# Kernel tuning notes

Hardware: AMD Instinct MI355X
Metric: run time of the kernel (lower is better)

## Reference

```python
import jax, jax.numpy as jnp
import numpy as np

# Dimensions (config.* values chosen per shape_source)
B, T, V = 64, 128, 512          # batch, seq_len, vocabnum (input feature dim)
H = 512                          # NUM_HIDDEN_UNITS
A = 64                           # ATTENTION_SIZE
C = 500                          # ClassEmbeddingsize
EPS = 1e-5


def _layer_norm(z, g, b):
    m = jnp.mean(z, axis=-1, keepdims=True)
    v = jnp.mean(jnp.square(z - m), axis=-1, keepdims=True)
    return (z - m) * jax.lax.rsqrt(v + EPS) * g + b


def _lstm_dir(x, w_ih, w_hh, ln_g, ln_b):
    # x: [T,B,D]; w_ih: [4H,D]; w_hh: [4H,H]; ln_g/ln_b: [9H] -> (ih 4H, hh 4H, cell H)
    g_ih, g_hh, g_c = ln_g[:4 * H], ln_g[4 * H:8 * H], ln_g[8 * H:]
    b_ih, b_hh, b_c = ln_b[:4 * H], ln_b[4 * H:8 * H], ln_b[8 * H:]
    # precompute input contribution for all steps, layer-normed over gate dim
    xg = _layer_norm(jnp.einsum('tbd,gd->tbg', x, w_ih), g_ih, b_ih)  # [T,B,4H]

    def step(carry, xg_t):
        h, c = carry
        gates = xg_t + _layer_norm(h @ w_hh.T, g_hh, b_hh)  # [B,4H]
        i, f, g, o = jnp.split(gates, 4, axis=-1)
        c = jax.nn.sigmoid(f) * c + jax.nn.sigmoid(i) * jnp.tanh(g)
        h = jax.nn.sigmoid(o) * jnp.tanh(_layer_norm(c, g_c, b_c))
        return (h, c), h

    h0 = jnp.zeros((x.shape[1], H), x.dtype)
    (_, _), hs = jax.lax.scan(step, (h0, h0), xg)
    return hs  # [T,B,H]


def _bilstm_layer(x, w_ih, w_hh, ln_g, ln_b):
    # direction-stacked params: w_ih [2,4H,D], w_hh [2,4H,H], ln_* [2,9H]
    fwd = _lstm_dir(x, w_ih[0], w_hh[0], ln_g[0], ln_b[0])
    bwd = _lstm_dir(x[::-1], w_ih[1], w_hh[1], ln_g[1], ln_b[1])[::-1]
    return jnp.concatenate([fwd, bwd], axis=-1)  # [T,B,2H]


def _batchnorm(x, g, b):
    # x: [B,C,L]; training-mode batch statistics over (B,L)
    m = jnp.mean(x, axis=(0, 2), keepdims=True)
    v = jnp.mean(jnp.square(x - m), axis=(0, 2), keepdims=True)
    return (x - m) * jax.lax.rsqrt(v + EPS) * g[None, :, None] + b[None, :, None]


def setup_inputs() -> dict:
    key = jax.random.key(0)
    ks = jax.random.split(key, 12)
    rn = lambda k, s: jax.random.normal(k, s, jnp.float32) * 0.05
    return {
        'batch_embedded': jax.random.normal(ks[0], (B, T, V), jnp.float32),
        'bn1_g': jnp.ones((V,), jnp.float32), 'bn1_b': jnp.zeros((V,), jnp.float32),
        'bn2_g': jnp.ones((2 * H,), jnp.float32), 'bn2_b': jnp.zeros((2 * H,), jnp.float32),
        'w_ih0': rn(ks[1], (2, 4 * H, V)), 'w_hh0': rn(ks[2], (2, 4 * H, H)),
        'lng0': jnp.ones((2, 9 * H), jnp.float32), 'lnb0': jnp.zeros((2, 9 * H), jnp.float32),
        'w_ih1': rn(ks[3], (2, 4 * H, 2 * H)), 'w_hh1': rn(ks[4], (2, 4 * H, H)),
        'lng1': jnp.ones((2, 9 * H), jnp.float32), 'lnb1': jnp.zeros((2, 9 * H), jnp.float32),
        'w_omega': rn(ks[5], (2 * H, A)), 'b_omega': rn(ks[6], (A,)), 'u_omega': rn(ks[7], (A,)),
        'W': jax.random.uniform(ks[8], (2 * H + 1, C + 1), jnp.float32) * 0.05,
    }


def reference(batch_embedded, bn1_g, bn1_b, bn2_g, bn2_b,
              w_ih0, w_hh0, lng0, lnb0, w_ih1, w_hh1, lng1, lnb1,
              w_omega, b_omega, u_omega, W):
    # BatchNorm1d over feature channels (dropout = identity in eval)
    x = _batchnorm(jnp.transpose(batch_embedded, (0, 2, 1)), bn1_g, bn1_b)  # [B,V,T]
    x = jnp.transpose(x, (2, 0, 1))  # [T,B,V]
    # 2-layer bidirectional layer-norm LSTM
    x = _bilstm_layer(x, w_ih0, w_hh0, lng0, lnb0)   # [T,B,2H]
    x = _bilstm_layer(x, w_ih1, w_hh1, lng1, lnb1)   # [T,B,2H]
    x = _batchnorm(jnp.transpose(x, (1, 2, 0)), bn2_g, bn2_b)  # [B,2H,T]
    x = jnp.transpose(x, (0, 2, 1))  # [B,T,2H]
    # Attention pooling over time
    v = jnp.tanh(x @ w_omega + b_omega)              # [B,T,A]
    alphas = jax.nn.softmax(v @ u_omega, axis=1)     # [B,T]
    pooled = jnp.sum(x * alphas[..., None], axis=1)  # [B,2H]
    emb = jnp.pad(pooled, ((0, 0), (0, 1)), constant_values=1.0)  # [B,2H+1]
    return emb @ W  # [B,C+1]
```

## Files before the change

kernel.cpp:

```cpp
#include <hip/hip_runtime.h>
#include <hip/hip_bf16.h>

#define LN_EPS 1e-5f

using bf16x8 = __attribute__((ext_vector_type(8))) short;
using f32x4  = __attribute__((ext_vector_type(4))) float;

__device__ __forceinline__ float bf2f(ushort u) {
    union { unsigned int i; float f; } v; v.i = ((unsigned int)u) << 16; return v.f;
}
__device__ __forceinline__ ushort f2bf(float f) {
    union { unsigned int i; float f; } v; v.f = f;
    unsigned int r = v.i + 0x7FFFu + ((v.i >> 16) & 1u);
    return (ushort)(r >> 16);
}
__device__ __forceinline__ void split3(float x, ushort& a, ushort& b, ushort& c) {
    a = f2bf(x); float r = x - bf2f(a);
    b = f2bf(r); float r2 = r - bf2f(b);
    c = f2bf(r2);
}

__device__ __forceinline__ unsigned ld_flag(const unsigned* p) {
    return __hip_atomic_load(p, __ATOMIC_RELAXED, __HIP_MEMORY_SCOPE_AGENT);
}
__device__ __forceinline__ void st_flag(unsigned* p, unsigned v) {
    __hip_atomic_store(p, v, __ATOMIC_RELAXED, __HIP_MEMORY_SCOPE_AGENT);
}

__device__ __forceinline__ void blockReduceSum2(float& a, float& b, float* red) {
    #pragma unroll
    for (int off = 32; off > 0; off >>= 1) {
        a += __shfl_down(a, off, 64);
        b += __shfl_down(b, off, 64);
    }
    const int nw = blockDim.x >> 6;
    const int w = threadIdx.x >> 6;
    if ((threadIdx.x & 63) == 0) { red[2 * w] = a; red[2 * w + 1] = b; }
    __syncthreads();
    if (threadIdx.x == 0) {
        float sa = 0.f, sb = 0.f;
        for (int i = 0; i < nw; ++i) { sa += red[2 * i]; sb += red[2 * i + 1]; }
        red[10] = sa; red[11] = sb;
    }
    __syncthreads();
    a = red[10]; b = red[11];
    __syncthreads();
}

__global__ __launch_bounds__(256) void conv_split3_k(const float* __restrict__ src, ushort* __restrict__ d0,
                                                     ushort* __restrict__ d1, ushort* __restrict__ d2, int n4) {
    int i = blockIdx.x * 256 + threadIdx.x;
    if (i < n4) {
        float4 v = ((const float4*)src)[i];
        ushort4 a, b, c;
        split3(v.x, a.x, b.x, c.x); split3(v.y, a.y, b.y, c.y);
        split3(v.z, a.z, b.z, c.z); split3(v.w, a.w, b.w, c.w);
        ((ushort4*)d0)[i] = a; ((ushort4*)d1)[i] = b; ((ushort4*)d2)[i] = c;
    }
}

__global__ __launch_bounds__(256) void bn1_stats_k(const float* __restrict__ in, float* __restrict__ st) {
    int b = blockIdx.x, tid = threadIdx.x;
    float s10 = 0, s20 = 0, s11 = 0, s21 = 0;
    const float* p = in + (size_t)b * 128 * 512;
    for (int t = 0; t < 128; ++t) {
        float x0 = p[t * 512 + tid];
        float x1 = p[t * 512 + tid + 256];
        s10 += x0; s20 += x0 * x0; s11 += x1; s21 += x1 * x1;
    }
    atomicAdd(&st[tid], s10);       atomicAdd(&st[512 + tid], s20);
    atomicAdd(&st[tid + 256], s11); atomicAdd(&st[512 + tid + 256], s21);
}

__global__ void bn1_final_k(const float* __restrict__ st, const float* __restrict__ g,
                            const float* __restrict__ bb, float* __restrict__ ac) {
    int d = threadIdx.x + blockIdx.x * 256;
    if (d < 512) {
        float m = st[d] * (1.f / 8192.f);
        float v = st[512 + d] * (1.f / 8192.f) - m * m;
        float a = g[d] * rsqrtf(v + LN_EPS);
        ac[d] = a; ac[512 + d] = bb[d] - m * a;
    }
}

__global__ __launch_bounds__(128) void bn1_apply3_k(const float* __restrict__ in, const float* __restrict__ ac,
                                                    ushort* __restrict__ x0, ushort* __restrict__ x1,
                                                    ushort* __restrict__ x2) {
    int beta = blockIdx.x;
    int t = beta >> 6, b = beta & 63;
    const float* src = in + ((size_t)b * 128 + t) * 512;
    #pragma unroll
    for (int k = 0; k < 4; ++k) {
        int d = threadIdx.x + 128 * k;
        ushort a, m, l;
        split3(ac[d] * src[d] + ac[512 + d], a, m, l);
        x0[(size_t)beta * 512 + d] = a;
        x1[(size_t)beta * 512 + d] = m;
        x2[(size_t)beta * 512 + d] = l;
    }
}

__global__ __launch_bounds__(256) void gemm6_k(const ushort* __restrict__ A0, const ushort* __restrict__ A1,
                                               const ushort* __restrict__ A2,
                                               const ushort* __restrict__ W0, const ushort* __restrict__ W1,
                                               const ushort* __restrict__ W2,
                                               float* __restrict__ C, int K) {
    const int dir = blockIdx.z;
    const ushort* Wp0 = W0 + (size_t)dir * 2048 * K;
    const ushort* Wp1 = W1 + (size_t)dir * 2048 * K;
    const ushort* Wp2 = W2 + (size_t)dir * 2048 * K;
    const int wave = threadIdx.x >> 6, lane = threadIdx.x & 63;
    const int l15 = lane & 15, kq = lane >> 4;
    const int m0 = blockIdx.y * 128 + (wave >> 1) * 64;
    const int n0 = blockIdx.x * 128 + (wave & 1) * 64;
    f32x4 acc[4][4];
    #pragma unroll
    for (int i = 0; i < 4; ++i)
        #pragma unroll
        for (int j = 0; j < 4; ++j) acc[i][j] = (f32x4){0.f, 0.f, 0.f, 0.f};
    for (int k0 = 0; k0 < K; k0 += 32) {
        bf16x8 a0[4], a1[4], a2[4], b0[4], b1[4], b2[4];
        #pragma unroll
        for (int i = 0; i < 4; ++i) {
            size_t o = (size_t)(m0 + i * 16 + l15) * K + k0 + kq * 8;
            a0[i] = *(const bf16x8*)(A0 + o);
            a1[i] = *(const bf16x8*)(A1 + o);
            a2[i] = *(const bf16x8*)(A2 + o);
        }
        #pragma unroll
        for (int j = 0; j < 4; ++j) {
            size_t o = (size_t)(n0 + j * 16 + l15) * K + k0 + kq * 8;
            b0[j] = *(const bf16x8*)(Wp0 + o);
            b1[j] = *(const bf16x8*)(Wp1 + o);
            b2[j] = *(const bf16x8*)(Wp2 + o);
        }
        #pragma unroll
        for (int i = 0; i < 4; ++i)
            #pragma unroll
            for (int j = 0; j < 4; ++j) {
                acc[i][j] = __builtin_amdgcn_mfma_f32_16x16x32_bf16(a2[i], b0[j], acc[i][j], 0, 0, 0);
                acc[i][j] = __builtin_amdgcn_mfma_f32_16x16x32_bf16(a1[i], b1[j], acc[i][j], 0, 0, 0);
                acc[i][j] = __builtin_amdgcn_mfma_f32_16x16x32_bf16(a0[i], b2[j], acc[i][j], 0, 0, 0);
                acc[i][j] = __builtin_amdgcn_mfma_f32_16x16x32_bf16(a1[i], b0[j], acc[i][j], 0, 0, 0);
                acc[i][j] = __builtin_amdgcn_mfma_f32_16x16x32_bf16(a0[i], b1[j], acc[i][j], 0, 0, 0);
                acc[i][j] = __builtin_amdgcn_mfma_f32_16x16x32_bf16(a0[i], b0[j], acc[i][j], 0, 0, 0);
            }
    }
    #pragma unroll
    for (int i = 0; i < 4; ++i)
        #pragma unroll
        for (int j = 0; j < 4; ++j)
            #pragma unroll
            for (int r = 0; r < 4; ++r)
                C[(size_t)dir * 8192 * 2048 + (size_t)(m0 + i * 16 + kq * 4 + r) * 2048 + n0 + j * 16 + l15]
                    = acc[i][j][r];
}

__global__ __launch_bounds__(256) void ln_rows32_k(float* __restrict__ X, const float* __restrict__ lng,
                                                   const float* __restrict__ lnb) {
    __shared__ float red[12];
    const int dir = blockIdx.y;
    float* row = X + ((size_t)dir * 8192 + blockIdx.x) * 2048;
    const float* g = lng + dir * 4608;
    const float* bb = lnb + dir * 4608;
    const int tid = threadIdx.x;
    float4 v0 = ((const float4*)row)[tid], v1 = ((const float4*)row)[tid + 256];
    float s1 = v0.x + v0.y + v0.z + v0.w + v1.x + v1.y + v1.z + v1.w;
    float s2 = v0.x * v0.x + v0.y * v0.y + v0.z * v0.z + v0.w * v0.w
             + v1.x * v1.x + v1.y * v1.y + v1.z * v1.z + v1.w * v1.w;
    blockReduceSum2(s1, s2, red);
    float m = s1 * (1.f / 2048.f);
    float rs = rsqrtf(s2 * (1.f / 2048.f) - m * m + LN_EPS);
    float4 g0 = ((const float4*)g)[tid],  g1 = ((const float4*)g)[tid + 256];
    float4 b0 = ((const float4*)bb)[tid], b1 = ((const float4*)bb)[tid + 256];
    float4 o0, o1;
    o0.x = (v0.x - m) * rs * g0.x + b0.x; o0.y = (v0.y - m) * rs * g0.y + b0.y;
    o0.z = (v0.z - m) * rs * g0.z + b0.z; o0.w = (v0.w - m) * rs * g0.w + b0.w;
    o1.x = (v1.x - m) * rs * g1.x + b1.x; o1.y = (v1.y - m) * rs * g1.y + b1.y;
    o1.z = (v1.z - m) * rs * g1.z + b1.z; o1.w = (v1.w - m) * rs * g1.w + b1.w;
    ((float4*)row)[tid] = o0;
    ((float4*)row)[tid + 256] = o1;
}

__device__ __forceinline__ void gbar3(unsigned int* flags, unsigned int e) {
    __builtin_amdgcn_s_waitcnt(0);
    __syncthreads();
    if (threadIdx.x == 0) {
        __builtin_amdgcn_fence(__ATOMIC_RELEASE, "agent");
        st_flag(&flags[blockIdx.x * 16], e);
    }
    if (threadIdx.x < 128) {
        while (ld_flag(&flags[threadIdx.x * 16]) < e)
            __builtin_amdgcn_s_sleep(2);
    }
    __syncthreads();
    __builtin_amdgcn_fence(__ATOMIC_ACQUIRE, "agent");
}

__global__ __launch_bounds__(256, 1) void lstm_scan5_k(
    const float* __restrict__ xg,
    const ushort* __restrict__ w0, const ushort* __restrict__ w1, const ushort* __restrict__ w2,
    const float* __restrict__ lng, const float* __restrict__ lnb,
    ushort* __restrict__ hb0, ushort* __restrict__ hb1, ushort* __restrict__ hb2,
    float* __restrict__ graw,
    ushort* __restrict__ hs0, ushort* __restrict__ hs1, ushort* __restrict__ hs2,
    unsigned int* __restrict__ flags) {
    __shared__ float red[12];
    const int beta = blockIdx.x, tid = threadIdx.x;
    const int dirB = beta >> 6, bB = beta & 63;
    const int wave = tid >> 6, lane = tid & 63, l15 = lane & 15, kq = lane >> 4;
    const size_t hro = (size_t)(dirB * 64 + bB) * 512;
    ((unsigned*)(hb0 + hro))[tid] = 0u;
    ((unsigned*)(hb1 + hro))[tid] = 0u;
    ((unsigned*)(hb2 + hro))[tid] = 0u;
    float c0 = 0.f, c1 = 0.f;
    const float* g_hh = lng + dirB * 4608 + 2048;
    const float* b_hh = lnb + dirB * 4608 + 2048;
    const float2 gcv = ((const float2*)(lng + dirB * 4608 + 4096))[tid];
    const float2 bcv = ((const float2*)(lnb + dirB * 4608 + 4096))[tid];
    const int jj = wave >> 1, ip = wave & 1;
    const int nn = bB * 32 + jj * 16;
    const ushort* h0d = hb0 + (size_t)dirB * 64 * 512;
    const ushort* h1d = hb1 + (size_t)dirB * 64 * 512;
    const ushort* h2d = hb2 + (size_t)dirB * 64 * 512;
    float* gr = graw + dirB * 64 * 2048;
    bf16x8 wr[16][3];
    {
        const ushort* w0d = w0 + (size_t)dirB * 2048 * 512;
        const ushort* w1d = w1 + (size_t)dirB * 2048 * 512;
        const ushort* w2d = w2 + (size_t)dirB * 2048 * 512;
        #pragma unroll
        for (int kt = 0; kt < 16; ++kt) {
            size_t wo = (size_t)(nn + l15) * 512 + kt * 32 + kq * 8;
            wr[kt][0] = *(const bf16x8*)(w0d + wo);
            wr[kt][1] = *(const bf16x8*)(w1d + wo);
            wr[kt][2] = *(const bf16x8*)(w2d + wo);
        }
    }
    unsigned int e = 0;
    gbar3(flags, ++e);
    for (int s = 0; s < 128; ++s) {
        {
            f32x4 acc[2];
            acc[0] = (f32x4){0.f, 0.f, 0.f, 0.f};
            acc[1] = (f32x4){0.f, 0.f, 0.f, 0.f};
            #pragma unroll
            for (int kt = 0; kt < 16; ++kt) {
                #pragma unroll
                for (int ii = 0; ii < 2; ++ii) {
                    size_t ho = (size_t)(ip * 32 + ii * 16 + l15) * 512 + kt * 32 + kq * 8;
                    bf16x8 a0 = *(const bf16x8*)(h0d + ho);
                    bf16x8 a1 = *(const bf16x8*)(h1d + ho);
                    bf16x8 a2 = *(const bf16x8*)(h2d + ho);
                    acc[ii] = __builtin_amdgcn_mfma_f32_16x16x32_bf16(a2, wr[kt][0], acc[ii], 0, 0, 0);
                    acc[ii] = __builtin_amdgcn_mfma_f32_16x16x32_bf16(a1, wr[kt][1], acc[ii], 0, 0, 0);
                    acc[ii] = __builtin_amdgcn_mfma_f32_16x16x32_bf16(a0, wr[kt][2], acc[ii], 0, 0, 0);
                    acc[ii] = __builtin_amdgcn_mfma_f32_16x16x32_bf16(a1, wr[kt][0], acc[ii], 0, 0, 0);
                    acc[ii] = __builtin_amdgcn_mfma_f32_16x16x32_bf16(a0, wr[kt][1], acc[ii], 0, 0, 0);
                    acc[ii] = __builtin_amdgcn_mfma_f32_16x16x32_bf16(a0, wr[kt][0], acc[ii], 0, 0, 0);
                }
            }
            #pragma unroll
            for (int ii = 0; ii < 2; ++ii)
                #pragma unroll
                for (int r = 0; r < 4; ++r)
                    gr[(ip * 32 + ii * 16 + kq * 4 + r) * 2048 + nn + l15] = acc[ii][r];
        }
        gbar3(flags, ++e);
        {
            const int time = dirB ? (127 - s) : s;
            const float2* grow = (const float2*)(gr + bB * 2048);
            float v[8];
            #pragma unroll
            for (int j = 0; j < 4; ++j) {
                float2 g2 = grow[j * 256 + tid];
                v[2 * j] = g2.x; v[2 * j + 1] = g2.y;
            }
            float s1 = 0.f, s2 = 0.f;
            #pragma unroll
            for (int k = 0; k < 8; ++k) { s1 += v[k]; s2 += v[k] * v[k]; }
            blockReduceSum2(s1, s2, red);
            float mu = s1 * (1.f / 2048.f);
            float rs = rsqrtf(s2 * (1.f / 2048.f) - mu * mu + LN_EPS);
            const float2* xr = (const float2*)(xg + ((size_t)dirB * 8192 + (size_t)time * 64 + bB) * 2048);
            float nv[8];
            #pragma unroll
            for (int j = 0; j < 4; ++j) {
                float2 xv = xr[tid + 256 * j];
                float2 gh = ((const float2*)g_hh)[tid + 256 * j];
                float2 bh = ((const float2*)b_hh)[tid + 256 * j];
                nv[2 * j]     = xv.x + (v[2 * j]     - mu) * rs * gh.x + bh.x;
                nv[2 * j + 1] = xv.y + (v[2 * j + 1] - mu) * rs * gh.y + bh.y;
            }
            float si0 = 1.f / (1.f + expf(-nv[0])), si1 = 1.f / (1.f + expf(-nv[1]));
            float sf0 = 1.f / (1.f + expf(-nv[2])), sf1 = 1.f / (1.f + expf(-nv[3]));
            c0 = sf0 * c0 + si0 * tanhf(nv[4]);
            c1 = sf1 * c1 + si1 * tanhf(nv[5]);
            float t1 = c0 + c1, t2 = c0 * c0 + c1 * c1;
            blockReduceSum2(t1, t2, red);
            float mc = t1 * (1.f / 512.f);
            float rc = rsqrtf(t2 * (1.f / 512.f) - mc * mc + LN_EPS);
            float so0 = 1.f / (1.f + expf(-nv[6])), so1 = 1.f / (1.f + expf(-nv[7]));
            float h0v = so0 * tanhf((c0 - mc) * rc * gcv.x + bcv.x);
            float h1v = so1 * tanhf((c1 - mc) * rc * gcv.y + bcv.y);
            ushort a0, m0, l0, a1, m1, l1;
            split3(h0v, a0, m0, l0);
            split3(h1v, a1, m1, l1);
            unsigned p0 = (unsigned)a0 | ((unsigned)a1 << 16);
            unsigned p1 = (unsigned)m0 | ((unsigned)m1 << 16);
            unsigned p2 = (unsigned)l0 | ((unsigned)l1 << 16);
            ((unsigned*)(hb0 + hro))[tid] = p0;
            ((unsigned*)(hb1 + hro))[tid] = p1;
            ((unsigned*)(hb2 + hro))[tid] = p2;
            size_t oro = ((size_t)time * 64 + bB) * 1024 + dirB * 512;
            ((unsigned*)(hs0 + oro))[tid] = p0;
            ((unsigned*)(hs1 + oro))[tid] = p1;
            ((unsigned*)(hs2 + oro))[tid] = p2;
        }
        gbar3(flags, ++e);
    }
}

__global__ __launch_bounds__(256) void bn2_stats3_k(const ushort* __restrict__ h0, const ushort* __restrict__ h1,
                                                    const ushort* __restrict__ h2, float* __restrict__ st) {
    int t = blockIdx.x, tid = threadIdx.x;
    float s1[4] = {0, 0, 0, 0}, s2[4] = {0, 0, 0, 0};
    size_t base = (size_t)t * 64 * 1024;
    for (int b = 0; b < 64; ++b) {
        #pragma unroll
        for (int k = 0; k < 4; ++k) {
            size_t o = base + b * 1024 + tid + 256 * k;
            float x = bf2f(h0[o]) + bf2f(h1[o]) + bf2f(h2[o]);
            s1[k] += x; s2[k] += x * x;
        }
    }
    #pragma unroll
    for (int k = 0; k < 4; ++k) {
        atomicAdd(&st[tid + 256 * k], s1[k]);
        atomicAdd(&st[1024 + tid + 256 * k], s2[k]);
    }
}

__global__ void bn2_final_k(const float* __restrict__ st, const float* __restrict__ g,
                            const float* __restrict__ bb, float* __restrict__ ac) {
    #pragma unroll
    for (int k = 0; k < 4; ++k) {
        int h = threadIdx.x + 256 * k;
        float m = st[h] * (1.f / 8192.f);
        float v = st[1024 + h] * (1.f / 8192.f) - m * m;
        float a = g[h] * rsqrtf(v + LN_EPS);
        ac[h] = a; ac[1024 + h] = bb[h] - m * a;
    }
}

__global__ __launch_bounds__(256) void bn2_apply3_k(const ushort* __restrict__ h0, const ushort* __restrict__ h1,
                                                    const ushort* __restrict__ h2, const float* __restrict__ ac,
                                                    float* __restrict__ y) {
    int beta = blockIdx.x;
    int b = beta >> 7, t = beta & 127;
    size_t so = ((size_t)t * 64 + b) * 1024;
    float* dst = y + (size_t)beta * 1024;
    #pragma unroll
    for (int k = 0; k < 4; ++k) {
        int h = threadIdx.x + 256 * k;
        float x = bf2f(h0[so + h]) + bf2f(h1[so + h]) + bf2f(h2[so + h]);
        dst[h] = ac[h] * x + ac[1024 + h];
    }
}

__global__ __launch_bounds__(64) void att_scores_k(const float* __restrict__ y, const float* __restrict__ wo,
                                                   const float* __restrict__ bo, const float* __restrict__ uo,
                                                   float* __restrict__ sc) {
    int row = blockIdx.x;
    int a = threadIdx.x;
    const float* yr = y + (size_t)row * 1024;
    float acc = bo[a];
    for (int h = 0; h < 1024; h += 4) {
        float4 yv = *(const float4*)(yr + h);
        acc += yv.x * wo[(h + 0) * 64 + a];
        acc += yv.y * wo[(h + 1) * 64 + a];
        acc += yv.z * wo[(h + 2) * 64 + a];
        acc += yv.w * wo[(h + 3) * 64 + a];
    }
    float p = tanhf(acc) * uo[a];
    #pragma unroll
    for (int off = 32; off > 0; off >>= 1) p += __shfl_down(p, off, 64);
    if (a == 0) sc[row] = p;
}

__global__ __launch_bounds__(128) void att_softmax_k(const float* __restrict__ sc, float* __restrict__ al) {
    __shared__ float red[8];
    int b = blockIdx.x, t = threadIdx.x;
    int lane = t & 63, w = t >> 6;
    float v = sc[b * 128 + t];
    float m = v;
    #pragma unroll
    for (int off = 32; off > 0; off >>= 1) m = fmaxf(m, __shfl_down(m, off, 64));
    if (lane == 0) red[w] = m;
    __syncthreads();
    m = fmaxf(red[0], red[1]);
    float e = expf(v - m);
    float sum = e;
    #pragma unroll
    for (int off = 32; off > 0; off >>= 1) sum += __shfl_down(sum, off, 64);
    if (lane == 0) red[2 + w] = sum;
    __syncthreads();
    sum = red[2] + red[3];
    al[b * 128 + t] = e / sum;
}

__global__ __launch_bounds__(256) void att_pool_k(const float* __restrict__ y, const float* __restrict__ al,
                                                  float* __restrict__ pooled) {
    int b = blockIdx.x, tid = threadIdx.x;
    float acc[4] = {0, 0, 0, 0};
    const float* yb = y + (size_t)b * 128 * 1024;
    for (int t = 0; t < 128; ++t) {
        float a = al[b * 128 + t];
        #pragma unroll
        for (int k = 0; k < 4; ++k) acc[k] += a * yb[t * 1024 + tid + 256 * k];
    }
    #pragma unroll
    for (int k = 0; k < 4; ++k) pooled[b * 1024 + tid + 256 * k] = acc[k];
}

__global__ __launch_bounds__(256) void out_gemv_k(const float* __restrict__ pooled, const float* __restrict__ W,
                                                  float* __restrict__ out) {
    int b = blockIdx.x, tid = threadIdx.x;
    const float* pb = pooled + b * 1024;
    #pragma unroll
    for (int rep = 0; rep < 2; ++rep) {
        int c = tid + rep * 256;
        if (c < 501) {
            float acc = W[(size_t)1024 * 501 + c];
            for (int h = 0; h < 1024; ++h) acc += pb[h] * W[(size_t)h * 501 + c];
            out[b * 501 + c] = acc;
        }
    }
}

extern "C" void kernel_launch(void* const* d_in, const int* in_sizes, int n_in,
                              void* d_out, int out_size, void* d_ws, size_t ws_size,
                              hipStream_t stream) {
    (void)in_sizes; (void)n_in; (void)out_size; (void)ws_size;
    const float* in_x  = (const float*)d_in[0];
    const float* bn1g  = (const float*)d_in[1];
    const float* bn1b  = (const float*)d_in[2];
    const float* bn2g  = (const float*)d_in[3];
    const float* bn2b  = (const float*)d_in[4];
    const float* w_ih0 = (const float*)d_in[5];
    const float* w_hh0 = (const float*)d_in[6];
    const float* lng0  = (const float*)d_in[7];
    const float* lnb0  = (const float*)d_in[8];
    const float* w_ih1 = (const float*)d_in[9];
    const float* w_hh1 = (const float*)d_in[10];
    const float* lng1  = (const float*)d_in[11];
    const float* lnb1  = (const float*)d_in[12];
    const float* w_om  = (const float*)d_in[13];
    const float* b_om  = (const float*)d_in[14];
    const float* u_om  = (const float*)d_in[15];
    const float* Wf    = (const float*)d_in[16];
    float* out = (float*)d_out;

    char* ws = (char*)d_ws;
    size_t off = 0;
    auto alloc = [&](size_t bytes) { size_t o = off; off += (bytes + 255) & ~(size_t)255; return o; };
    float*  xg     = (float*)(ws + alloc(2ull * 8192 * 2048 * 4));
    ushort* hs0_0  = (ushort*)(ws + alloc(8192ull * 1024 * 2));
    ushort* hs0_1  = (ushort*)(ws + alloc(8192ull * 1024 * 2));
    ushort* hs0_2  = (ushort*)(ws + alloc(8192ull * 1024 * 2));
    char*   hs1reg = ws + alloc(3ull * 8192 * 1024 * 2);
    ushort* WH1_0  = (ushort*)(ws + alloc(2ull * 2048 * 512 * 2));
    ushort* WH1_1  = (ushort*)(ws + alloc(2ull * 2048 * 512 * 2));
    ushort* WH1_2  = (ushort*)(ws + alloc(2ull * 2048 * 512 * 2));
    float*  graw   = (float*)(ws + alloc(2ull * 64 * 2048 * 4));
    ushort* hb0    = (ushort*)(ws + alloc(2ull * 64 * 512 * 2));
    ushort* hb1    = (ushort*)(ws + alloc(2ull * 64 * 512 * 2));
    ushort* hb2    = (ushort*)(ws + alloc(2ull * 64 * 512 * 2));
    float*  st1    = (float*)(ws + alloc(1024 * 4));
    float*  ac1    = (float*)(ws + alloc(1024 * 4));
    float*  st2    = (float*)(ws + alloc(2048 * 4));
    float*  ac2    = (float*)(ws + alloc(2048 * 4));
    float*  sc     = (float*)(ws + alloc(8192 * 4));
    float*  al     = (float*)(ws + alloc(8192 * 4));
    float*  pooled = (float*)(ws + alloc(64ull * 1024 * 4));
    unsigned int* bar0 = (unsigned int*)(ws + alloc(128 * 16 * 4));
    unsigned int* bar1 = (unsigned int*)(ws + alloc(128 * 16 * 4));
    ushort* hs1_0 = (ushort*)hs1reg;
    ushort* hs1_1 = (ushort*)(hs1reg + 16777216);
    ushort* hs1_2 = (ushort*)(hs1reg + 33554432);
    ushort* xn0   = (ushort*)(hs1reg + 0);
    ushort* xn1   = (ushort*)(hs1reg + 8388608);
    ushort* xn2   = (ushort*)(hs1reg + 16777216);
    ushort* WI0_0 = (ushort*)(hs1reg + 25165824);
    ushort* WI0_1 = (ushort*)(hs1reg + 29360128);
    ushort* WI0_2 = (ushort*)(hs1reg + 33554432);
    ushort* WH0_0 = (ushort*)(hs1reg + 37748736);
    ushort* WH0_1 = (ushort*)(hs1reg + 41943040);
    ushort* WH0_2 = (ushort*)(hs1reg + 46137344);
    ushort* WI1_0 = (ushort*)(hs1reg + 0);
    ushort* WI1_1 = (ushort*)(hs1reg + 8388608);
    ushort* WI1_2 = (ushort*)(hs1reg + 16777216);
    float*  ybuf  = (float*)xg;

    hipMemsetAsync(st1, 0, 1024 * 4, stream);
    hipMemsetAsync(st2, 0, 2048 * 4, stream);
    hipMemsetAsync(bar0, 0, 128 * 16 * 4, stream);
    hipMemsetAsync(bar1, 0, 128 * 16 * 4, stream);

    conv_split3_k<<<2048, 256, 0, stream>>>(w_ih0, WI0_0, WI0_1, WI0_2, 2097152 / 4);
    conv_split3_k<<<2048, 256, 0, stream>>>(w_hh0, WH0_0, WH0_1, WH0_2, 2097152 / 4);

    bn1_stats_k<<<64, 256, 0, stream>>>(in_x, st1);
    bn1_final_k<<<2, 256, 0, stream>>>(st1, bn1g, bn1b, ac1);
    bn1_apply3_k<<<8192, 128, 0, stream>>>(in_x, ac1, xn0, xn1, xn2);

    gemm6_k<<<dim3(16, 64, 2), 256, 0, stream>>>(xn0, xn1, xn2, WI0_0, WI0_1, WI0_2, xg, 512);
    ln_rows32_k<<<dim3(8192, 2), 256, 0, stream>>>(xg, lng0, lnb0);
    lstm_scan5_k<<<128, 256, 0, stream>>>(xg, WH0_0, WH0_1, WH0_2, lng0, lnb0,
                                          hb0, hb1, hb2, graw, hs0_0, hs0_1, hs0_2, bar0);

    conv_split3_k<<<4096, 256, 0, stream>>>(w_ih1, WI1_0, WI1_1, WI1_2, 4194304 / 4);
    conv_split3_k<<<2048, 256, 0, stream>>>(w_hh1, WH1_0, WH1_1, WH1_2, 2097152 / 4);

    gemm6_k<<<dim3(16, 64, 2), 256, 0, stream>>>(hs0_0, hs0_1, hs0_2, WI1_0, WI1_1, WI1_2, xg, 1024);
    ln_rows32_k<<<dim3(8192, 2), 256, 0, stream>>>(xg, lng1, lnb1);
    lstm_scan5_k<<<128, 256, 0, stream>>>(xg, WH1_0, WH1_1, WH1_2, lng1, lnb1,
                                          hb0, hb1, hb2, graw, hs1_0, hs1_1, hs1_2, bar1);

    bn2_stats3_k<<<128, 256, 0, stream>>>(hs1_0, hs1_1, hs1_2, st2);
    bn2_final_k<<<1, 256, 0, stream>>>(st2, bn2g, bn2b, ac2);
    bn2_apply3_k<<<8192, 256, 0, stream>>>(hs1_0, hs1_1, hs1_2, ac2, ybuf);

    att_scores_k<<<8192, 64, 0, stream>>>(ybuf, w_om, b_om, u_om, sc);
    att_softmax_k<<<64, 128, 0, stream>>>(sc, al);
    att_pool_k<<<64, 256, 0, stream>>>(ybuf, al, pooled);
    out_gemv_k<<<64, 256, 0, stream>>>(pooled, Wf, out);
}
```

Measured before the change: 8.829 ms.

## Split grid barrier per direction and use coherent atomics instead of fences

Each grid barrier now waits only on the 64 blocks of its own LSTM direction instead of all 128. The release fence before the flag store is removed. Cross-block data (graw, h buffers) is now written and read with relaxed agent-scope atomic loads and stores, so the acquire fence is kept only on the barrier after the h update. The xg row load for the step is also hoisted above the matmul so its latency overlaps compute. This reduces barrier and fence cost on the serial recurrence, but memory ordering now rests on the atomic accesses without an explicit release fence, which is a correctness risk.

```diff
diff --git a/kernel.cpp b/kernel.cpp
--- a/kernel.cpp
+++ b/kernel.cpp
@@ -25,6 +25,15 @@
 }
 __device__ __forceinline__ void st_flag(unsigned* p, unsigned v) {
     __hip_atomic_store(p, v, __ATOMIC_RELAXED, __HIP_MEMORY_SCOPE_AGENT);
+}
+__device__ __forceinline__ unsigned long long ld_u64_c(const void* p) {
+    return __hip_atomic_load((const unsigned long long*)p, __ATOMIC_RELAXED, __HIP_MEMORY_SCOPE_AGENT);
+}
+__device__ __forceinline__ void st_u32_c(void* p, unsigned v) {
+    __hip_atomic_store((unsigned*)p, v, __ATOMIC_RELAXED, __HIP_MEMORY_SCOPE_AGENT);
+}
+__device__ __forceinline__ void st_f32_c(void* p, float v) {
+    union { unsigned u; float f; } c; c.f = v; st_u32_c(p, c.u);
 }
 
 __device__ __forceinline__ void blockReduceSum2(float& a, float& b, float* red) {
@@ -182,22 +191,22 @@
     ((float4*)row)[tid + 256] = o1;
 }
 
-__device__ __forceinline__ void gbar3(unsigned int* flags, unsigned int e) {
+template <bool INV>
+__device__ __forceinline__ void gbar4(unsigned int* flags, int dirB, unsigned e) {
     __builtin_amdgcn_s_waitcnt(0);
     __syncthreads();
-    if (threadIdx.x == 0) {
-        __builtin_amdgcn_fence(__ATOMIC_RELEASE, "agent");
+    if (threadIdx.x == 0)
         st_flag(&flags[blockIdx.x * 16], e);
-    }
-    if (threadIdx.x < 128) {
-        while (ld_flag(&flags[threadIdx.x * 16]) < e)
+    if (threadIdx.x < 64) {
+        while (ld_flag(&flags[(dirB * 64 + threadIdx.x) * 16]) < e)
             __builtin_amdgcn_s_sleep(2);
     }
     __syncthreads();
-    __builtin_amdgcn_fence(__ATOMIC_ACQUIRE, "agent");
-}
-
-__global__ __launch_bounds__(256, 1) void lstm_scan5_k(
+    if (INV)
+        __builtin_amdgcn_fence(__ATOMIC_ACQUIRE, "agent");
+}
+
+__global__ __launch_bounds__(256, 1) void lstm_scan6_k(
     const float* __restrict__ xg,
     const ushort* __restrict__ w0, const ushort* __restrict__ w1, const ushort* __restrict__ w2,
     const float* __restrict__ lng, const float* __restrict__ lnb,
@@ -210,9 +219,9 @@
     const int dirB = beta >> 6, bB = beta & 63;
     const int wave = tid >> 6, lane = tid & 63, l15 = lane & 15, kq = lane >> 4;
     const size_t hro = (size_t)(dirB * 64 + bB) * 512;
-    ((unsigned*)(hb0 + hro))[tid] = 0u;
-    ((unsigned*)(hb1 + hro))[tid] = 0u;
-    ((unsigned*)(hb2 + hro))[tid] = 0u;
+    st_u32_c((unsigned*)(hb0 + hro) + tid, 0u);
+    st_u32_c((unsigned*)(hb1 + hro) + tid, 0u);
+    st_u32_c((unsigned*)(hb2 + hro) + tid, 0u);
     float c0 = 0.f, c1 = 0.f;
     const float* g_hh = lng + dirB * 4608 + 2048;
     const float* b_hh = lnb + dirB * 4608 + 2048;
@@ -238,8 +247,13 @@
         }
     }
     unsigned int e = 0;
-    gbar3(flags, ++e);
+    gbar4<true>(flags, dirB, ++e);
     for (int s = 0; s < 128; ++s) {
+        const int time = dirB ? (127 - s) : s;
+        const float2* xr = (const float2*)(xg + ((size_t)dirB * 8192 + (size_t)time * 64 + bB) * 2048);
+        float2 xv[4];
+        #pragma unroll
+        for (int j = 0; j < 4; ++j) xv[j] = xr[tid + 256 * j];
         {
             f32x4 acc[2];
             acc[0] = (f32x4){0.f, 0.f, 0.f, 0.f};
@@ -264,17 +278,18 @@
             for (int ii = 0; ii < 2; ++ii)
                 #pragma unroll
                 for (int r = 0; r < 4; ++r)
-                    gr[(ip * 32 + ii * 16 + kq * 4 + r) * 2048 + nn + l15] = acc[ii][r];
-        }
-        gbar3(flags, ++e);
+                    st_f32_c(&gr[(ip * 32 + ii * 16 + kq * 4 + r) * 2048 + nn + l15], acc[ii][r]);
+        }
+        gbar4<false>(flags, dirB, ++e);
         {
-            const int time = dirB ? (127 - s) : s;
-            const float2* grow = (const float2*)(gr + bB * 2048);
+            const float* grow = gr + bB * 2048;
+            const int base = 2 * tid;
             float v[8];
             #pragma unroll
             for (int j = 0; j < 4; ++j) {
-                float2 g2 = grow[j * 256 + tid];
-                v[2 * j] = g2.x; v[2 * j + 1] = g2.y;
+                union { unsigned long long q; float f[2]; } c;
+                c.q = ld_u64_c(&grow[j * 512 + base]);
+                v[2 * j] = c.f[0]; v[2 * j + 1] = c.f[1];
             }
             float s1 = 0.f, s2 = 0.f;
             #pragma unroll
@@ -282,15 +297,13 @@
             blockReduceSum2(s1, s2, red);
             float mu = s1 * (1.f / 2048.f);
             float rs = rsqrtf(s2 * (1.f / 2048.f) - mu * mu + LN_EPS);
-            const float2* xr = (const float2*)(xg + ((size_t)dirB * 8192 + (size_t)time * 64 + bB) * 2048);
             float nv[8];
             #pragma unroll
             for (int j = 0; j < 4; ++j) {
-                float2 xv = xr[tid + 256 * j];
                 float2 gh = ((const float2*)g_hh)[tid + 256 * j];
                 float2 bh = ((const float2*)b_hh)[tid + 256 * j];
-                nv[2 * j]     = xv.x + (v[2 * j]     - mu) * rs * gh.x + bh.x;
-                nv[2 * j + 1] = xv.y + (v[2 * j + 1] - mu) * rs * gh.y + bh.y;
+                nv[2 * j]     = xv[j].x + (v[2 * j]     - mu) * rs * gh.x + bh.x;
+                nv[2 * j + 1] = xv[j].y + (v[2 * j + 1] - mu) * rs * gh.y + bh.y;
             }
             float si0 = 1.f / (1.f + expf(-nv[0])), si1 = 1.f / (1.f + expf(-nv[1]));
             float sf0 = 1.f / (1.f + expf(-nv[2])), sf1 = 1.f / (1.f + expf(-nv[3]));
@@ -309,15 +322,15 @@
             unsigned p0 = (unsigned)a0 | ((unsigned)a1 << 16);
             unsigned p1 = (unsigned)m0 | ((unsigned)m1 << 16);
             unsigned p2 = (unsigned)l0 | ((unsigned)l1 << 16);
-            ((unsigned*)(hb0 + hro))[tid] = p0;
-            ((unsigned*)(hb1 + hro))[tid] = p1;
-            ((unsigned*)(hb2 + hro))[tid] = p2;
+            st_u32_c((unsigned*)(hb0 + hro) + tid, p0);
+            st_u32_c((unsigned*)(hb1 + hro) + tid, p1);
+            st_u32_c((unsigned*)(hb2 + hro) + tid, p2);
             size_t oro = ((size_t)time * 64 + bB) * 1024 + dirB * 512;
             ((unsigned*)(hs0 + oro))[tid] = p0;
             ((unsigned*)(hs1 + oro))[tid] = p1;
             ((unsigned*)(hs2 + oro))[tid] = p2;
         }
-        gbar3(flags, ++e);
+        gbar4<true>(flags, dirB, ++e);
     }
 }
 
@@ -516,7 +529,7 @@
 
     gemm6_k<<<dim3(16, 64, 2), 256, 0, stream>>>(xn0, xn1, xn2, WI0_0, WI0_1, WI0_2, xg, 512);
     ln_rows32_k<<<dim3(8192, 2), 256, 0, stream>>>(xg, lng0, lnb0);
-    lstm_scan5_k<<<128, 256, 0, stream>>>(xg, WH0_0, WH0_1, WH0_2, lng0, lnb0,
+    lstm_scan6_k<<<128, 256, 0, stream>>>(xg, WH0_0, WH0_1, WH0_2, lng0, lnb0,
                                           hb0, hb1, hb2, graw, hs0_0, hs0_1, hs0_2, bar0);
 
     conv_split3_k<<<4096, 256, 0, stream>>>(w_ih1, WI1_0, WI1_1, WI1_2, 4194304 / 4);
@@ -524,7 +537,7 @@
 
     gemm6_k<<<dim3(16, 64, 2), 256, 0, stream>>>(hs0_0, hs0_1, hs0_2, WI1_0, WI1_1, WI1_2, xg, 1024);
     ln_rows32_k<<<dim3(8192, 2), 256, 0, stream>>>(xg, lng1, lnb1);
-    lstm_scan5_k<<<128, 256, 0, stream>>>(xg, WH1_0, WH1_1, WH1_2, lng1, lnb1,
+    lstm_scan6_k<<<128, 256, 0, stream>>>(xg, WH1_0, WH1_1, WH1_2, lng1, lnb1,
                                           hb0, hb1, hb2, graw, hs1_0, hs1_1, hs1_2, bar1);
 
     bn2_stats3_k<<<128, 256, 0, stream>>>(hs1_0, hs1_1, hs1_2, st2);
```

New measurement: 7.783 ms. -11.8%, faster.
